# Optimization experiments

Hardware: AMD Instinct MI355X
Metric: run time of the kernel (lower is better)

## Reference

```python
import jax, jax.numpy as jnp
import numpy as np

B, T, I, H, F = 32, 1024, 64, 512, 63
NEG = -1e9


def _init_params(key):
    ks = jax.random.split(key, 16)
    s = 0.02
    p = {}
    # LSTM (pytorch gate order i,f,g,o)
    p['w_ih'] = jax.random.normal(ks[0], (4 * H, I), jnp.float32) * s
    p['w_hh'] = jax.random.normal(ks[1], (4 * H, H), jnp.float32) * s
    p['b_ih'] = jnp.zeros((4 * H,), jnp.float32)
    p['b_hh'] = jnp.zeros((4 * H,), jnp.float32)
    # shared layer
    p['w_sh'] = jax.random.normal(ks[2], (H, H), jnp.float32) * s
    p['b_sh'] = jnp.zeros((H,), jnp.float32)
    # state attention: Linear(H,H) -> tanh -> Linear(H,1)
    p['w_sa'] = jax.random.normal(ks[3], (H, H), jnp.float32) * s
    p['b_sa'] = jnp.zeros((H,), jnp.float32)
    p['v_sa'] = jax.random.normal(ks[4], (1, H), jnp.float32) * s
    p['bv_sa'] = jnp.zeros((1,), jnp.float32)
    # reward attention
    p['w_ra'] = jax.random.normal(ks[5], (H, H), jnp.float32) * s
    p['b_ra'] = jnp.zeros((H,), jnp.float32)
    p['v_ra'] = jax.random.normal(ks[6], (1, H), jnp.float32) * s
    p['bv_ra'] = jnp.zeros((1,), jnp.float32)
    # heads
    p['w_st'] = jax.random.normal(ks[7], (F, H), jnp.float32) * s
    p['b_st'] = jnp.zeros((F,), jnp.float32)
    p['w_rw'] = jax.random.normal(ks[8], (1, H), jnp.float32) * s
    p['b_rw'] = jnp.zeros((1,), jnp.float32)
    return p


def setup_inputs() -> dict:
    key = jax.random.key(0)
    k1, k2, k3, kp = jax.random.split(key, 4)
    inp = {
        'x': jax.random.normal(k1, (B, T, I), jnp.float32),
        'x_lengths': jnp.full((B,), T, dtype=jnp.int64),  # full lengths: pack/pad is identity
        'h0': jax.random.normal(k2, (B, H), jnp.float32),
        'c0': jax.random.normal(k3, (B, H), jnp.float32),
    }
    inp.update(_init_params(kp))
    return inp


def _lstm(x, h0, c0, w_ih, w_hh, b_ih, b_hh):
    # x: [B,T,I] -> outputs [B,T,H], final (h,c)
    def step(carry, xt):
        h, c = carry
        gates = xt @ w_ih.T + h @ w_hh.T + b_ih + b_hh  # [B,4H]
        i, f, g, o = jnp.split(gates, 4, axis=-1)
        c = jax.nn.sigmoid(f) * c + jax.nn.sigmoid(i) * jnp.tanh(g)
        h = jax.nn.sigmoid(o) * jnp.tanh(c)
        return (h, c), h
    (hT, cT), outs = jax.lax.scan(step, (h0, c0), jnp.swapaxes(x, 0, 1))
    return jnp.swapaxes(outs, 0, 1), hT, cT


def _causal_attn(feat, w1, b1, v, bv):
    # additive attention pooling over every causal prefix, vectorized over t.
    e = jnp.tanh(feat @ w1.T + b1) @ v.T + bv        # [B,T,1]
    e = e[..., 0]                                     # [B,T]
    t = feat.shape[1]
    causal = jnp.tril(jnp.ones((t, t), bool))         # [T,T] j<=t
    logits = jnp.where(causal[None], e[:, None, :], NEG)
    w = jax.nn.softmax(logits, axis=-1)               # [B,T,T]
    return jnp.einsum('btj,bjh->bth', w, feat)        # [B,T,H]


def reference(x, x_lengths, h0, c0, w_ih, w_hh, b_ih, b_hh, w_sh, b_sh,
              w_sa, b_sa, v_sa, bv_sa, w_ra, b_ra, v_ra, bv_ra,
              w_st, b_st, w_rw, b_rw):
    r_out, hT, cT = _lstm(x, h0, c0, w_ih, w_hh, b_ih, b_hh)
    shared = r_out @ w_sh.T + b_sh                    # [B,T,H]
    state_ctx = _causal_attn(shared, w_sa, b_sa, v_sa, bv_sa)
    reward_ctx = _causal_attn(shared, w_ra, b_ra, v_ra, bv_ra)
    state_outs = state_ctx @ w_st.T + b_st            # [B,T,F]
    reward_outs = reward_ctx @ w_rw.T + b_rw          # [B,T,1]
    return state_outs, reward_outs, (hT, cT)
```

## Files before the change

### kernel.cpp

```cpp
#include <hip/hip_runtime.h>

#define BB 32
#define TT 1024
#define II 64
#define HH 512
#define FF 63
#define G4H 2048
#define KK 576
#define MM 32768

#define RW_OFF 2064384
#define HT_OFF 2097152
#define CT_OFF 2113536

#define WS_FLAGS   0
#define WS_FLAG    4096
#define WS_TICK    4224
#define WS_CHOSEN  4288
#define WS_BIASC   4352
#define WS_BSH     12544
#define WS_BCSA    14592
#define WS_BCRA    16640
#define WS_BCH     18688
#define WS_SCAL    18944
#define WS_VS      19072
#define WS_VR      20096
#define WS_ZB      21120
#define WS_H0      23168
#define WS_CP      88704
#define WS_WHPAD   121472
#define WS_WHC     252544
#define WS_WSHT    383616
#define WS_WSA     907904
#define WS_WRA     1432192
#define WS_WCSA    1956480
#define WS_WCRA    2480768
#define WS_WCAT    3005056
#define WS_XP      5364352
#define WS_ES      9558656
#define WS_ER      9689728
#define WS_PROJ    9820800
#define WS_HX      14015104

typedef __bf16  bf16x8 __attribute__((ext_vector_type(8)));
typedef float   f32x4  __attribute__((ext_vector_type(4)));
typedef unsigned int u32x4v __attribute__((ext_vector_type(4)));
typedef uint4 uint4a __attribute__((may_alias));
typedef unsigned int u32;

#define POLL_SENTINEL 0x7FFFFFFFu

__device__ __forceinline__ float bf2f(unsigned short u) {
    unsigned int v = ((unsigned int)u) << 16;
    return __builtin_bit_cast(float, v);
}
__device__ __forceinline__ unsigned short f2bf(float f) {
    unsigned int u = __builtin_bit_cast(unsigned int, f);
    u += 0x7fffu + ((u >> 16) & 1u);
    return (unsigned short)(u >> 16);
}
__device__ __forceinline__ bf16x8 ldb8(const unsigned short* p) {
    uint4 v = *(const uint4a*)p;
    return __builtin_bit_cast(bf16x8, v);
}
__device__ __forceinline__ float sigf(float x) { return 1.f / (1.f + __expf(-x)); }
__device__ __forceinline__ float tanhfast(float x) { return 1.f - 2.f / (__expf(2.f * x) + 1.f); }

__device__ __forceinline__ unsigned short loadu(const void* p, int i, int fl) {
    return fl ? f2bf(((const float*)p)[i]) : ((const unsigned short*)p)[i];
}
__device__ __forceinline__ float loadf(const void* p, int i, int fl) {
    return fl ? ((const float*)p)[i] : bf2f(((const unsigned short*)p)[i]);
}

__global__ void sniff_k(const unsigned short* __restrict__ xr, unsigned int* __restrict__ flag) {
    if (threadIdx.x == 0) {
        int cnt = 0;
        for (int i = 0; i < 256; ++i) {
            unsigned short u = xr[i];
            int e = (u >> 7) & 0xFF;
            if (u == 0 || (e >= 100 && e <= 140)) ++cnt;
        }
        *flag = (cnt < 220) ? 1u : 0u;
    }
}

__global__ void prep_all(const void* x, const void* h0, const void* c0,
                         const void* w_sh, const void* w_sa, const void* w_ra,
                         const void* w_st, const void* w_rw,
                         const void* v_sa, const void* v_ra,
                         const void* b_sh, const void* bv_sa, const void* bv_ra,
                         char* ws) {
    const int fl = (int)*(const unsigned int*)(ws + WS_FLAG);
    unsigned short* xp    = (unsigned short*)(ws + WS_XP);
    unsigned short* h0s   = (unsigned short*)(ws + WS_H0);
    unsigned short* cp    = (unsigned short*)(ws + WS_CP);
    unsigned short* wshT  = (unsigned short*)(ws + WS_WSHT);
    unsigned short* wsa   = (unsigned short*)(ws + WS_WSA);
    unsigned short* wra   = (unsigned short*)(ws + WS_WRA);
    unsigned short* whpad = (unsigned short*)(ws + WS_WHPAD);
    unsigned short* vs    = (unsigned short*)(ws + WS_VS);
    unsigned short* vr    = (unsigned short*)(ws + WS_VR);
    float* bsh  = (float*)(ws + WS_BSH);
    float* scal = (float*)(ws + WS_SCAL);
    float* zb   = (float*)(ws + WS_ZB);

    int gt = blockIdx.x * 256 + threadIdx.x;
    int gs = gridDim.x * 256;
    for (int i = gt; i < BB * TT * II; i += gs) xp[i] = loadu(x, i, fl);
    for (int i = gt; i < BB * HH; i += gs) { h0s[i] = loadu(h0, i, fl); cp[i] = loadu(c0, i, fl); }
    for (int i = gt; i < HH * HH; i += gs) {
        int m = i >> 9, k = i & 511;
        wshT[k * HH + m] = loadu(w_sh, i, fl);
        wsa[i] = loadu(w_sa, i, fl);
        wra[i] = loadu(w_ra, i, fl);
    }
    for (int i = gt; i < 128 * HH; i += gs) {
        int f = i >> 9, k = i & 511;
        whpad[i] = (f < FF) ? loadu(w_st, f * HH + k, fl)
                 : (f == FF ? loadu(w_rw, k, fl) : (unsigned short)0);
    }
    for (int i = gt; i < HH; i += gs) {
        vs[i] = loadu(v_sa, i, fl); vr[i] = loadu(v_ra, i, fl);
        bsh[i] = loadf(b_sh, i, fl); zb[i] = 0.f;
    }
    if (gt == 0) { scal[0] = loadf(bv_sa, 0, fl); scal[1] = loadf(bv_ra, 0, fl); }
}

__global__ void prep_w(const void* __restrict__ w_hh, const void* __restrict__ w_ih,
                       const void* __restrict__ b_ih, const void* __restrict__ b_hh,
                       char* ws) {
    const int fl = (int)*(const unsigned int*)(ws + WS_FLAG);
    unsigned short* wcat = (unsigned short*)(ws + WS_WCAT);
    float* biasc = (float*)(ws + WS_BIASC);
    int c = blockIdx.x;
    for (int k = threadIdx.x; k < KK; k += 256)
        wcat[c * KK + k] = (k < HH) ? loadu(w_hh, c * HH + k, fl)
                                    : loadu(w_ih, c * II + (k - HH), fl);
    if (threadIdx.x == 0) biasc[c] = loadf(b_ih, c, fl) + loadf(b_hh, c, fl);
}

__global__ void bias_comb(const void* b_sa, const void* b_ra,
                          const void* b_st, const void* b_rw, char* ws) {
    const int fl = (int)*(const unsigned int*)(ws + WS_FLAG);
    const float* bsh = (const float*)(ws + WS_BSH);
    int j = threadIdx.x;
    if (blockIdx.x == 0) {
        const unsigned short* w = (const unsigned short*)(ws + WS_WSA);
        float s = loadf(b_sa, j, fl);
        for (int k = 0; k < HH; ++k) s += bf2f(w[j * HH + k]) * bsh[k];
        ((float*)(ws + WS_BCSA))[j] = s;
    } else if (blockIdx.x == 1) {
        const unsigned short* w = (const unsigned short*)(ws + WS_WRA);
        float s = loadf(b_ra, j, fl);
        for (int k = 0; k < HH; ++k) s += bf2f(w[j * HH + k]) * bsh[k];
        ((float*)(ws + WS_BCRA))[j] = s;
    } else if (j < 64) {
        const unsigned short* w = (const unsigned short*)(ws + WS_WHPAD);
        float s = (j < FF) ? loadf(b_st, j, fl) : loadf(b_rw, 0, fl);
        for (int k = 0; k < HH; ++k) s += bf2f(w[j * HH + k]) * bsh[k];
        ((float*)(ws + WS_BCH))[j] = s;
    }
}

__global__ void init_e(char* ws) {
    const float* scal = (const float*)(ws + WS_SCAL);
    float* es = (float*)(ws + WS_ES);
    float* er = (float*)(ws + WS_ER);
    int i = blockIdx.x * 256 + threadIdx.x;
    if (i < MM) { es[i] = scal[0]; er[i] = scal[1]; }
}

__global__ __launch_bounds__(256, 1)
void lstm_k(char* __restrict__ ws, void* __restrict__ dout) {
    __shared__ float gbuf[32][68];
    __shared__ int s_slot;
    __shared__ int s_dead;

    u32* tick   = (u32*)(ws + WS_TICK);
    u32* chosen = (u32*)(ws + WS_CHOSEN);

    if (threadIdx.x == 0) {
        u32 xcc;
        asm volatile("s_getreg_b32 %0, hwreg(HW_REG_XCC_ID)" : "=s"(xcc));
        xcc &= 7u;
        int slot = -1;
        u32 tk = __hip_atomic_fetch_add(&tick[xcc], 1u, __ATOMIC_RELAXED,
                                        __HIP_MEMORY_SCOPE_AGENT);
        if (tk < (u32)BB) {
            if (tk == (u32)BB - 1u) {
                u32 expected = 0u;
                __hip_atomic_compare_exchange_strong(chosen, &expected, xcc + 1u,
                    __ATOMIC_RELAXED, __ATOMIC_RELAXED, __HIP_MEMORY_SCOPE_AGENT);
            }
            u32 c = 0u;
            for (int it = 0; it < (1 << 20); ++it) {
                c = __hip_atomic_load(chosen, __ATOMIC_RELAXED, __HIP_MEMORY_SCOPE_AGENT);
                if (c != 0u) break;
                __builtin_amdgcn_s_sleep(8);
            }
            if (c == xcc + 1u) slot = (int)tk;
        }
        s_slot = slot;
        s_dead = 0;
    }
    __syncthreads();
    const int g = s_slot;
    if (g < 0) return;

    const unsigned short* xp    = (const unsigned short*)(ws + WS_XP);
    const unsigned short* wcat  = (const unsigned short*)(ws + WS_WCAT);
    const float*          biasc = (const float*)(ws + WS_BIASC);
    const unsigned short* cinit = (const unsigned short*)(ws + WS_CP);
    const unsigned short* h0s   = (const unsigned short*)(ws + WS_H0);
    unsigned short*       hx    = (unsigned short*)(ws + WS_HX);
    u32*                  flags = (u32*)(ws + WS_FLAGS);
    const int fl = (int)*(const unsigned int*)(ws + WS_FLAG);

    const int tid  = threadIdx.x;
    const int wave = tid >> 6, lane = tid & 63;
    const int quad = lane >> 4, l16 = lane & 15;
    const int mh = wave & 1, nh = wave >> 1;
    const int m = mh * 16 + l16;

    bf16x8 bw[2][18];
#pragma unroll
    for (int tn = 0; tn < 2; ++tn) {
        int nl   = nh * 32 + tn * 16 + l16;
        int gcol = (nl >> 4) * HH + g * 16 + (nl & 15);
        const unsigned short* wp = wcat + gcol * KK + quad * 8;
#pragma unroll
        for (int ks = 0; ks < 18; ++ks) bw[tn][ks] = ldb8(wp + ks * 32);
    }
#pragma unroll
    for (int tn = 0; tn < 2; ++tn)
#pragma unroll
        for (int ks = 0; ks < 18; ++ks) {
            u32x4v tmp = __builtin_bit_cast(u32x4v, bw[tn][ks]);
            asm volatile("" : "+v"(tmp));
            bw[tn][ks] = __builtin_bit_cast(bf16x8, tmp);
        }

    const int b  = tid >> 3, pr = tid & 7, cc = pr * 2;
    const int n  = g * 16 + cc;
    const float bi0 = biasc[n],          bi1 = biasc[n + 1];
    const float bff0 = biasc[HH + n],    bff1 = biasc[HH + n + 1];
    const float bg0 = biasc[2*HH + n],   bg1 = biasc[2*HH + n + 1];
    const float bo0 = biasc[3*HH + n],   bo1 = biasc[3*HH + n + 1];
    float cst0 = bf2f(cinit[b * HH + n]);
    float cst1 = bf2f(cinit[b * HH + n + 1]);

    const unsigned short* xbase = xp + m * (TT * II) + quad * 8;
    bf16x8 ax0 = ldb8(xbase), ax1 = ldb8(xbase + 32);

    u32* myflag = flags + g * 32;
    u32* pollp  = flags + (lane & 31) * 32;

    for (int t = 0; t < TT; ++t) {
        int tn1 = (t + 1 < TT) ? t + 1 : t;
        bf16x8 axn0 = ldb8(xbase + tn1 * II);
        bf16x8 axn1 = ldb8(xbase + tn1 * II + 32);

        const unsigned short* hrow =
            (t == 0 ? h0s : hx + (t - 1) * (BB * HH)) + m * HH + quad * 8;
        bf16x8 a[16];
#pragma unroll
        for (int i = 0; i < 16; ++i) a[i] = ldb8(hrow + i * 32);

        f32x4 acc0 = {0.f, 0.f, 0.f, 0.f}, acc1 = {0.f, 0.f, 0.f, 0.f};
#pragma unroll
        for (int i = 0; i < 16; ++i) {
            acc0 = __builtin_amdgcn_mfma_f32_16x16x32_bf16(a[i], bw[0][i], acc0, 0, 0, 0);
            acc1 = __builtin_amdgcn_mfma_f32_16x16x32_bf16(a[i], bw[1][i], acc1, 0, 0, 0);
        }
        acc0 = __builtin_amdgcn_mfma_f32_16x16x32_bf16(ax0, bw[0][16], acc0, 0, 0, 0);
        acc1 = __builtin_amdgcn_mfma_f32_16x16x32_bf16(ax0, bw[1][16], acc1, 0, 0, 0);
        acc0 = __builtin_amdgcn_mfma_f32_16x16x32_bf16(ax1, bw[0][17], acc0, 0, 0, 0);
        acc1 = __builtin_amdgcn_mfma_f32_16x16x32_bf16(ax1, bw[1][17], acc1, 0, 0, 0);

        {
            int row = mh * 16 + quad * 4;
#pragma unroll
            for (int r = 0; r < 4; ++r) gbuf[row + r][nh * 32 + l16]      = acc0[r];
#pragma unroll
            for (int r = 0; r < 4; ++r) gbuf[row + r][nh * 32 + 16 + l16] = acc1[r];
        }
        __syncthreads();

        {
            float2 giv = *(const float2*)&gbuf[b][cc];
            float2 gfv = *(const float2*)&gbuf[b][16 + cc];
            float2 ggv = *(const float2*)&gbuf[b][32 + cc];
            float2 gov = *(const float2*)&gbuf[b][48 + cc];
            cst0 = sigf(gfv.x + bff0) * cst0 + sigf(giv.x + bi0) * tanhfast(ggv.x + bg0);
            cst1 = sigf(gfv.y + bff1) * cst1 + sigf(giv.y + bi1) * tanhfast(ggv.y + bg1);
            float h0v = sigf(gov.x + bo0) * tanhfast(cst0);
            float h1v = sigf(gov.y + bo1) * tanhfast(cst1);
            u32 hp = (u32)f2bf(h0v) | ((u32)f2bf(h1v) << 16);
            *(u32*)&hx[t * (BB * HH) + b * HH + n] = hp;
            if (t == TT - 1) {
                if (fl) {
                    ((float*)dout)[HT_OFF + b * HH + n]     = h0v;
                    ((float*)dout)[HT_OFF + b * HH + n + 1] = h1v;
                    ((float*)dout)[CT_OFF + b * HH + n]     = cst0;
                    ((float*)dout)[CT_OFF + b * HH + n + 1] = cst1;
                } else {
                    ((u32*)dout)[(HT_OFF + b * HH + n) >> 1] = hp;
                    ((u32*)dout)[(CT_OFF + b * HH + n) >> 1] =
                        (u32)f2bf(cst0) | ((u32)f2bf(cst1) << 16);
                }
            }
        }
        __syncthreads();

        if (tid == 0)
            (void)__hip_atomic_fetch_add(myflag, 1u, __ATOMIC_RELAXED,
                                         __HIP_MEMORY_SCOPE_WORKGROUP);

        if (wave == 0) {
            u32 tgt = (u32)(t + 1);
            int trip = 0;
            for (int it = 0;; ++it) {
                u32 v = POLL_SENTINEL;
                __hip_atomic_compare_exchange_strong(pollp, &v, POLL_SENTINEL,
                    __ATOMIC_RELAXED, __ATOMIC_RELAXED, __HIP_MEMORY_SCOPE_WORKGROUP);
                if (__all((int)(v >= tgt && v != POLL_SENTINEL))) break;
                if (it > (1 << 16)) { trip = 1; break; }
                __builtin_amdgcn_s_sleep(1);
            }
            if (trip && lane == 0) s_dead = 1;
        }
        __syncthreads();
        if (s_dead) break;
        asm volatile("" ::: "memory");
        ax0 = axn0; ax1 = axn1;
    }
}

template <int EPI>
__global__ __launch_bounds__(256)
void gemm_bt(const unsigned short* __restrict__ A,
             const unsigned short* __restrict__ W,
             const float* __restrict__ bias,
             void* __restrict__ Cv, int N,
             const unsigned short* __restrict__ vv,
             float* __restrict__ eout) {
    __shared__ unsigned short As[128][72];
    __shared__ unsigned short Bs[64][72];
    const int tid = threadIdx.x;
    const int wave = tid >> 6, lane = tid & 63, quad = lane >> 4, l16 = lane & 15;
    const int mb = blockIdx.x, nb = blockIdx.y;

    f32x4 acc[2][4];
#pragma unroll
    for (int tm = 0; tm < 2; ++tm)
#pragma unroll
        for (int tn = 0; tn < 4; ++tn) acc[tm][tn] = (f32x4){0.f, 0.f, 0.f, 0.f};

    for (int k0 = 0; k0 < 512; k0 += 64) {
#pragma unroll
        for (int i = 0; i < 4; ++i) {
            int v = tid + i * 256;
            int rowa = v >> 3, kc = (v & 7) * 8;
            *(uint4a*)&As[rowa][kc] = *(const uint4a*)(A + (mb * 128 + rowa) * 512 + k0 + kc);
        }
#pragma unroll
        for (int i = 0; i < 2; ++i) {
            int v = tid + i * 256;
            int rowb = v >> 3, kc = (v & 7) * 8;
            *(uint4a*)&Bs[rowb][kc] = *(const uint4a*)(W + (nb * 64 + rowb) * 512 + k0 + kc);
        }
        __syncthreads();
#pragma unroll
        for (int ks = 0; ks < 2; ++ks) {
            bf16x8 a0 = ldb8(&As[wave * 32 + l16][ks * 32 + quad * 8]);
            bf16x8 a1 = ldb8(&As[wave * 32 + 16 + l16][ks * 32 + quad * 8]);
#pragma unroll
            for (int tn = 0; tn < 4; ++tn) {
                bf16x8 bb = ldb8(&Bs[tn * 16 + l16][ks * 32 + quad * 8]);
                acc[0][tn] = __builtin_amdgcn_mfma_f32_16x16x32_bf16(a0, bb, acc[0][tn], 0, 0, 0);
                acc[1][tn] = __builtin_amdgcn_mfma_f32_16x16x32_bf16(a1, bb, acc[1][tn], 0, 0, 0);
            }
        }
        __syncthreads();
    }
    if (EPI == 0) {
#pragma unroll
        for (int tm = 0; tm < 2; ++tm)
#pragma unroll
            for (int tn = 0; tn < 4; ++tn)
#pragma unroll
                for (int r = 0; r < 4; ++r) {
                    int row = mb * 128 + wave * 32 + tm * 16 + quad * 4 + r;
                    int col = nb * 64 + tn * 16 + l16;
                    ((unsigned short*)Cv)[row * N + col] = f2bf(acc[tm][tn][r] + bias[col]);
                }
    } else {
        float vcol[4], bcol[4];
#pragma unroll
        for (int tn = 0; tn < 4; ++tn) {
            int col = nb * 64 + tn * 16 + l16;
            vcol[tn] = bf2f(vv[col]); bcol[tn] = bias[col];
        }
#pragma unroll
        for (int tm = 0; tm < 2; ++tm)
#pragma unroll
            for (int r = 0; r < 4; ++r) {
                float s = 0.f;
#pragma unroll
                for (int tn = 0; tn < 4; ++tn)
                    s += vcol[tn] * tanhfast(acc[tm][tn][r] + bcol[tn]);
                s += __shfl_xor(s, 1); s += __shfl_xor(s, 2);
                s += __shfl_xor(s, 4); s += __shfl_xor(s, 8);
                if (l16 == 0) {
                    int row = mb * 128 + wave * 32 + tm * 16 + quad * 4 + r;
                    atomicAdd(&eout[row], s);
                }
            }
    }
}

__global__ __launch_bounds__(64)
void cumsum_k(char* __restrict__ ws, void* __restrict__ dout) {
    const unsigned short* proj = (const unsigned short*)(ws + WS_PROJ);
    const float* es = (const float*)(ws + WS_ES);
    const float* er = (const float*)(ws + WS_ER);
    const int fl = (int)*(const unsigned int*)(ws + WS_FLAG);
    const int b = blockIdx.x, lane = threadIdx.x;
    const bool isr = (lane == 63);
    float m_ = -3e38f, d_ = 0.f, n_ = 0.f;
    float pj = bf2f(proj[b * 64 + lane]);
    float e  = isr ? er[b] : es[b];
    for (int t = 0; t < TT; ++t) {
        float pjn = 0.f, en = 0.f;
        if (t + 1 < TT) {
            int rn = (t + 1) * BB + b;
            pjn = bf2f(proj[rn * 64 + lane]);
            en  = isr ? er[rn] : es[rn];
        }
        float mn = fmaxf(m_, e);
        float al = __expf(m_ - mn);
        float p  = __expf(e - mn);
        d_ = d_ * al + p;
        n_ = n_ * al + p * pj;
        m_ = mn;
        float o = n_ / d_;
        int rout = b * TT + t;
        int addr = isr ? (RW_OFF + rout) : (rout * FF + lane);
        if (fl) ((float*)dout)[addr] = o;
        else    ((unsigned short*)dout)[addr] = f2bf(o);
        pj = pjn; e = en;
    }
}

extern "C" void kernel_launch(void* const* d_in, const int* in_sizes, int n_in,
                              void* d_out, int out_size, void* d_ws, size_t ws_size,
                              hipStream_t stream) {
    const void* x    = d_in[0];
    const void* h0   = d_in[2];
    const void* c0   = d_in[3];
    const void* w_ih = d_in[4];
    const void* w_hh = d_in[5];
    const void* b_ih = d_in[6];
    const void* b_hh = d_in[7];
    const void* w_sh = d_in[8];
    const void* b_sh = d_in[9];
    const void* w_sa = d_in[10];
    const void* b_sa = d_in[11];
    const void* v_sa = d_in[12];
    const void* bv_sa= d_in[13];
    const void* w_ra = d_in[14];
    const void* b_ra = d_in[15];
    const void* v_ra = d_in[16];
    const void* bv_ra= d_in[17];
    const void* w_st = d_in[18];
    const void* b_st = d_in[19];
    const void* w_rw = d_in[20];
    const void* b_rw = d_in[21];

    char* ws = (char*)d_ws;
    unsigned short* wsa   = (unsigned short*)(ws + WS_WSA);
    unsigned short* wra   = (unsigned short*)(ws + WS_WRA);
    unsigned short* whpad = (unsigned short*)(ws + WS_WHPAD);
    unsigned short* wshT  = (unsigned short*)(ws + WS_WSHT);
    unsigned short* wcsa  = (unsigned short*)(ws + WS_WCSA);
    unsigned short* wcra  = (unsigned short*)(ws + WS_WCRA);
    unsigned short* whc   = (unsigned short*)(ws + WS_WHC);
    unsigned short* routs = (unsigned short*)(ws + WS_HX);
    unsigned short* proj  = (unsigned short*)(ws + WS_PROJ);
    unsigned short* vs    = (unsigned short*)(ws + WS_VS);
    unsigned short* vr    = (unsigned short*)(ws + WS_VR);
    float* zb   = (float*)(ws + WS_ZB);
    float* bcsa = (float*)(ws + WS_BCSA);
    float* bcra = (float*)(ws + WS_BCRA);
    float* bch  = (float*)(ws + WS_BCH);
    float* es   = (float*)(ws + WS_ES);
    float* er   = (float*)(ws + WS_ER);

    (void)hipMemsetAsync(d_ws, 0, 4352, stream);
    sniff_k<<<1, 64, 0, stream>>>((const unsigned short*)x, (unsigned int*)(ws + WS_FLAG));
    prep_all<<<1024, 256, 0, stream>>>(x, h0, c0, w_sh, w_sa, w_ra, w_st, w_rw,
                                       v_sa, v_ra, b_sh, bv_sa, bv_ra, ws);
    prep_w<<<G4H, 256, 0, stream>>>(w_hh, w_ih, b_ih, b_hh, ws);

    lstm_k<<<256, 256, 0, stream>>>(ws, d_out);

    gemm_bt<0><<<dim3(4, 8), 256, 0, stream>>>(wsa,   wshT, zb, wcsa, 512, nullptr, nullptr);
    gemm_bt<0><<<dim3(4, 8), 256, 0, stream>>>(wra,   wshT, zb, wcra, 512, nullptr, nullptr);
    gemm_bt<0><<<dim3(1, 8), 256, 0, stream>>>(whpad, wshT, zb, whc,  512, nullptr, nullptr);
    bias_comb<<<3, 512, 0, stream>>>(b_sa, b_ra, b_st, b_rw, ws);
    init_e<<<MM / 256, 256, 0, stream>>>(ws);

    gemm_bt<2><<<dim3(MM / 128, 8), 256, 0, stream>>>(routs, wcsa, bcsa, nullptr, 512, vs, es);
    gemm_bt<2><<<dim3(MM / 128, 8), 256, 0, stream>>>(routs, wcra, bcra, nullptr, 512, vr, er);
    gemm_bt<0><<<dim3(MM / 128, 1), 256, 0, stream>>>(routs, whc, bch, proj, 64, nullptr, nullptr);
    cumsum_k<<<BB, 64, 0, stream>>>(ws, d_out);
}
```

Before: 4.940 ms.

## Halve LSTM workgroups to 16 with wider column slices and merge attention GEMMs

The persistent LSTM now runs on 16 workgroups instead of 32, each computing 32 hidden units (128 gate columns) with four MFMA accumulators and twice the register-resident weights. This cuts the number of flag-polling peers in the per-step cross-workgroup barrier, removes the sleep in the poll loop, and signals a dead flag on timeout. Each thread now updates two cell pairs per step, so there is more serial work per workgroup and higher register pressure. The two attention-score GEMMs are merged into one launch with 16 column blocks, which relies on adjacent workspace layout of the weights, biases and score buffers. init_e is moved earlier in the launch order.

```diff
diff --git a/kernel.cpp b/kernel.cpp
--- a/kernel.cpp
+++ b/kernel.cpp
@@ -8,6 +8,7 @@
 #define G4H 2048
 #define KK 576
 #define MM 32768
+#define NW 16
 
 #define RW_OFF 2064384
 #define HT_OFF 2097152
@@ -44,7 +45,6 @@
 
 typedef __bf16  bf16x8 __attribute__((ext_vector_type(8)));
 typedef float   f32x4  __attribute__((ext_vector_type(4)));
-typedef unsigned int u32x4v __attribute__((ext_vector_type(4)));
 typedef uint4 uint4a __attribute__((may_alias));
 typedef unsigned int u32;
 
@@ -173,7 +173,7 @@
 
 __global__ __launch_bounds__(256, 1)
 void lstm_k(char* __restrict__ ws, void* __restrict__ dout) {
-    __shared__ float gbuf[32][68];
+    __shared__ float gbuf[32][132];
     __shared__ int s_slot;
     __shared__ int s_dead;
 
@@ -187,8 +187,8 @@
         int slot = -1;
         u32 tk = __hip_atomic_fetch_add(&tick[xcc], 1u, __ATOMIC_RELAXED,
                                         __HIP_MEMORY_SCOPE_AGENT);
-        if (tk < (u32)BB) {
-            if (tk == (u32)BB - 1u) {
+        if (tk < (u32)NW) {
+            if (tk == (u32)NW - 1u) {
                 u32 expected = 0u;
                 __hip_atomic_compare_exchange_strong(chosen, &expected, xcc + 1u,
                     __ATOMIC_RELAXED, __ATOMIC_RELAXED, __HIP_MEMORY_SCOPE_AGENT);
@@ -223,38 +223,35 @@
     const int mh = wave & 1, nh = wave >> 1;
     const int m = mh * 16 + l16;
 
-    bf16x8 bw[2][18];
-#pragma unroll
-    for (int tn = 0; tn < 2; ++tn) {
-        int nl   = nh * 32 + tn * 16 + l16;
-        int gcol = (nl >> 4) * HH + g * 16 + (nl & 15);
+    bf16x8 bw[4][18];
+#pragma unroll
+    for (int tn = 0; tn < 4; ++tn) {
+        int nl   = nh * 64 + tn * 16 + l16;
+        int gcol = (nl >> 5) * HH + g * 32 + (nl & 31);
         const unsigned short* wp = wcat + gcol * KK + quad * 8;
 #pragma unroll
         for (int ks = 0; ks < 18; ++ks) bw[tn][ks] = ldb8(wp + ks * 32);
     }
-#pragma unroll
-    for (int tn = 0; tn < 2; ++tn)
-#pragma unroll
-        for (int ks = 0; ks < 18; ++ks) {
-            u32x4v tmp = __builtin_bit_cast(u32x4v, bw[tn][ks]);
-            asm volatile("" : "+v"(tmp));
-            bw[tn][ks] = __builtin_bit_cast(bf16x8, tmp);
-        }
-
-    const int b  = tid >> 3, pr = tid & 7, cc = pr * 2;
-    const int n  = g * 16 + cc;
-    const float bi0 = biasc[n],          bi1 = biasc[n + 1];
-    const float bff0 = biasc[HH + n],    bff1 = biasc[HH + n + 1];
-    const float bg0 = biasc[2*HH + n],   bg1 = biasc[2*HH + n + 1];
-    const float bo0 = biasc[3*HH + n],   bo1 = biasc[3*HH + n + 1];
-    float cst0 = bf2f(cinit[b * HH + n]);
-    float cst1 = bf2f(cinit[b * HH + n + 1]);
+
+    const int b0 = tid >> 4,          cc0 = (tid & 15) * 2;
+    const int b1 = (tid + 256) >> 4,  cc1 = ((tid + 256) & 15) * 2;
+    const int n0 = g * 32 + cc0, n1 = g * 32 + cc1;
+    const float bi0a = biasc[n0],        bi0b = biasc[n0 + 1];
+    const float bf0a = biasc[HH + n0],   bf0b = biasc[HH + n0 + 1];
+    const float bg0a = biasc[2*HH + n0], bg0b = biasc[2*HH + n0 + 1];
+    const float bo0a = biasc[3*HH + n0], bo0b = biasc[3*HH + n0 + 1];
+    const float bi1a = biasc[n1],        bi1b = biasc[n1 + 1];
+    const float bf1a = biasc[HH + n1],   bf1b = biasc[HH + n1 + 1];
+    const float bg1a = biasc[2*HH + n1], bg1b = biasc[2*HH + n1 + 1];
+    const float bo1a = biasc[3*HH + n1], bo1b = biasc[3*HH + n1 + 1];
+    float cst0a = bf2f(cinit[b0 * HH + n0]), cst0b = bf2f(cinit[b0 * HH + n0 + 1]);
+    float cst1a = bf2f(cinit[b1 * HH + n1]), cst1b = bf2f(cinit[b1 * HH + n1 + 1]);
 
     const unsigned short* xbase = xp + m * (TT * II) + quad * 8;
     bf16x8 ax0 = ldb8(xbase), ax1 = ldb8(xbase + 32);
 
     u32* myflag = flags + g * 32;
-    u32* pollp  = flags + (lane & 31) * 32;
+    u32* pollp  = flags + (lane & (NW - 1)) * 32;
 
     for (int t = 0; t < TT; ++t) {
         int tn1 = (t + 1 < TT) ? t + 1 : t;
@@ -263,51 +260,82 @@
 
         const unsigned short* hrow =
             (t == 0 ? h0s : hx + (t - 1) * (BB * HH)) + m * HH + quad * 8;
-        bf16x8 a[16];
-#pragma unroll
-        for (int i = 0; i < 16; ++i) a[i] = ldb8(hrow + i * 32);
-
-        f32x4 acc0 = {0.f, 0.f, 0.f, 0.f}, acc1 = {0.f, 0.f, 0.f, 0.f};
-#pragma unroll
-        for (int i = 0; i < 16; ++i) {
-            acc0 = __builtin_amdgcn_mfma_f32_16x16x32_bf16(a[i], bw[0][i], acc0, 0, 0, 0);
-            acc1 = __builtin_amdgcn_mfma_f32_16x16x32_bf16(a[i], bw[1][i], acc1, 0, 0, 0);
-        }
-        acc0 = __builtin_amdgcn_mfma_f32_16x16x32_bf16(ax0, bw[0][16], acc0, 0, 0, 0);
-        acc1 = __builtin_amdgcn_mfma_f32_16x16x32_bf16(ax0, bw[1][16], acc1, 0, 0, 0);
-        acc0 = __builtin_amdgcn_mfma_f32_16x16x32_bf16(ax1, bw[0][17], acc0, 0, 0, 0);
-        acc1 = __builtin_amdgcn_mfma_f32_16x16x32_bf16(ax1, bw[1][17], acc1, 0, 0, 0);
+        f32x4 acc[4];
+#pragma unroll
+        for (int tn = 0; tn < 4; ++tn) acc[tn] = (f32x4){0.f, 0.f, 0.f, 0.f};
+#pragma unroll
+        for (int hf = 0; hf < 2; ++hf) {
+            bf16x8 a[8];
+#pragma unroll
+            for (int i = 0; i < 8; ++i) a[i] = ldb8(hrow + (hf * 8 + i) * 32);
+#pragma unroll
+            for (int i = 0; i < 8; ++i)
+#pragma unroll
+                for (int tn = 0; tn < 4; ++tn)
+                    acc[tn] = __builtin_amdgcn_mfma_f32_16x16x32_bf16(
+                        a[i], bw[tn][hf * 8 + i], acc[tn], 0, 0, 0);
+        }
+#pragma unroll
+        for (int tn = 0; tn < 4; ++tn) {
+            acc[tn] = __builtin_amdgcn_mfma_f32_16x16x32_bf16(ax0, bw[tn][16], acc[tn], 0, 0, 0);
+            acc[tn] = __builtin_amdgcn_mfma_f32_16x16x32_bf16(ax1, bw[tn][17], acc[tn], 0, 0, 0);
+        }
 
         {
             int row = mh * 16 + quad * 4;
 #pragma unroll
-            for (int r = 0; r < 4; ++r) gbuf[row + r][nh * 32 + l16]      = acc0[r];
-#pragma unroll
-            for (int r = 0; r < 4; ++r) gbuf[row + r][nh * 32 + 16 + l16] = acc1[r];
+            for (int tn = 0; tn < 4; ++tn)
+#pragma unroll
+                for (int r = 0; r < 4; ++r)
+                    gbuf[row + r][nh * 64 + tn * 16 + l16] = acc[tn][r];
         }
         __syncthreads();
 
         {
-            float2 giv = *(const float2*)&gbuf[b][cc];
-            float2 gfv = *(const float2*)&gbuf[b][16 + cc];
-            float2 ggv = *(const float2*)&gbuf[b][32 + cc];
-            float2 gov = *(const float2*)&gbuf[b][48 + cc];
-            cst0 = sigf(gfv.x + bff0) * cst0 + sigf(giv.x + bi0) * tanhfast(ggv.x + bg0);
-            cst1 = sigf(gfv.y + bff1) * cst1 + sigf(giv.y + bi1) * tanhfast(ggv.y + bg1);
-            float h0v = sigf(gov.x + bo0) * tanhfast(cst0);
-            float h1v = sigf(gov.y + bo1) * tanhfast(cst1);
-            u32 hp = (u32)f2bf(h0v) | ((u32)f2bf(h1v) << 16);
-            *(u32*)&hx[t * (BB * HH) + b * HH + n] = hp;
+            float2 gi = *(const float2*)&gbuf[b0][cc0];
+            float2 gf = *(const float2*)&gbuf[b0][32 + cc0];
+            float2 gg = *(const float2*)&gbuf[b0][64 + cc0];
+            float2 go = *(const float2*)&gbuf[b0][96 + cc0];
+            cst0a = sigf(gf.x + bf0a) * cst0a + sigf(gi.x + bi0a) * tanhfast(gg.x + bg0a);
+            cst0b = sigf(gf.y + bf0b) * cst0b + sigf(gi.y + bi0b) * tanhfast(gg.y + bg0b);
+            float ha = sigf(go.x + bo0a) * tanhfast(cst0a);
+            float hb = sigf(go.y + bo0b) * tanhfast(cst0b);
+            u32 hp = (u32)f2bf(ha) | ((u32)f2bf(hb) << 16);
+            *(u32*)&hx[t * (BB * HH) + b0 * HH + n0] = hp;
             if (t == TT - 1) {
                 if (fl) {
-                    ((float*)dout)[HT_OFF + b * HH + n]     = h0v;
-                    ((float*)dout)[HT_OFF + b * HH + n + 1] = h1v;
-                    ((float*)dout)[CT_OFF + b * HH + n]     = cst0;
-                    ((float*)dout)[CT_OFF + b * HH + n + 1] = cst1;
+                    ((float*)dout)[HT_OFF + b0 * HH + n0]     = ha;
+                    ((float*)dout)[HT_OFF + b0 * HH + n0 + 1] = hb;
+                    ((float*)dout)[CT_OFF + b0 * HH + n0]     = cst0a;
+                    ((float*)dout)[CT_OFF + b0 * HH + n0 + 1] = cst0b;
                 } else {
-                    ((u32*)dout)[(HT_OFF + b * HH + n) >> 1] = hp;
-                    ((u32*)dout)[(CT_OFF + b * HH + n) >> 1] =
-                        (u32)f2bf(cst0) | ((u32)f2bf(cst1) << 16);
+                    ((u32*)dout)[(HT_OFF + b0 * HH + n0) >> 1] = hp;
+                    ((u32*)dout)[(CT_OFF + b0 * HH + n0) >> 1] =
+                        (u32)f2bf(cst0a) | ((u32)f2bf(cst0b) << 16);
+                }
+            }
+        }
+        {
+            float2 gi = *(const float2*)&gbuf[b1][cc1];
+            float2 gf = *(const float2*)&gbuf[b1][32 + cc1];
+            float2 gg = *(const float2*)&gbuf[b1][64 + cc1];
+            float2 go = *(const float2*)&gbuf[b1][96 + cc1];
+            cst1a = sigf(gf.x + bf1a) * cst1a + sigf(gi.x + bi1a) * tanhfast(gg.x + bg1a);
+            cst1b = sigf(gf.y + bf1b) * cst1b + sigf(gi.y + bi1b) * tanhfast(gg.y + bg1b);
+            float ha = sigf(go.x + bo1a) * tanhfast(cst1a);
+            float hb = sigf(go.y + bo1b) * tanhfast(cst1b);
+            u32 hp = (u32)f2bf(ha) | ((u32)f2bf(hb) << 16);
+            *(u32*)&hx[t * (BB * HH) + b1 * HH + n1] = hp;
+            if (t == TT - 1) {
+                if (fl) {
+                    ((float*)dout)[HT_OFF + b1 * HH + n1]     = ha;
+                    ((float*)dout)[HT_OFF + b1 * HH + n1 + 1] = hb;
+                    ((float*)dout)[CT_OFF + b1 * HH + n1]     = cst1a;
+                    ((float*)dout)[CT_OFF + b1 * HH + n1 + 1] = cst1b;
+                } else {
+                    ((u32*)dout)[(HT_OFF + b1 * HH + n1) >> 1] = hp;
+                    ((u32*)dout)[(CT_OFF + b1 * HH + n1) >> 1] =
+                        (u32)f2bf(cst1a) | ((u32)f2bf(cst1b) << 16);
                 }
             }
         }
@@ -321,14 +349,20 @@
             u32 tgt = (u32)(t + 1);
             int trip = 0;
             for (int it = 0;; ++it) {
-                u32 v = POLL_SENTINEL;
-                __hip_atomic_compare_exchange_strong(pollp, &v, POLL_SENTINEL,
-                    __ATOMIC_RELAXED, __ATOMIC_RELAXED, __HIP_MEMORY_SCOPE_WORKGROUP);
+                u32 v = tgt;
+                if (lane < NW) {
+                    v = POLL_SENTINEL;
+                    __hip_atomic_compare_exchange_strong(pollp, &v, POLL_SENTINEL,
+                        __ATOMIC_RELAXED, __ATOMIC_RELAXED, __HIP_MEMORY_SCOPE_WORKGROUP);
+                }
                 if (__all((int)(v >= tgt && v != POLL_SENTINEL))) break;
-                if (it > (1 << 16)) { trip = 1; break; }
-                __builtin_amdgcn_s_sleep(1);
-            }
-            if (trip && lane == 0) s_dead = 1;
+                if (it > (1 << 13)) { trip = 1; break; }
+            }
+            if (trip && lane == 0) {
+                __hip_atomic_store(myflag, (u32)(TT + 2), __ATOMIC_RELAXED,
+                                   __HIP_MEMORY_SCOPE_WORKGROUP);
+                s_dead = 1;
+            }
         }
         __syncthreads();
         if (s_dead) break;
@@ -396,6 +430,7 @@
                     ((unsigned short*)Cv)[row * N + col] = f2bf(acc[tm][tn][r] + bias[col]);
                 }
     } else {
+        const int eoff = (nb >= 8) ? MM : 0;
         float vcol[4], bcol[4];
 #pragma unroll
         for (int tn = 0; tn < 4; ++tn) {
@@ -414,7 +449,7 @@
                 s += __shfl_xor(s, 4); s += __shfl_xor(s, 8);
                 if (l16 == 0) {
                     int row = mb * 128 + wave * 32 + tm * 16 + quad * 4 + r;
-                    atomicAdd(&eout[row], s);
+                    atomicAdd(&eout[eoff + row], s);
                 }
             }
     }
@@ -489,19 +524,17 @@
     unsigned short* routs = (unsigned short*)(ws + WS_HX);
     unsigned short* proj  = (unsigned short*)(ws + WS_PROJ);
     unsigned short* vs    = (unsigned short*)(ws + WS_VS);
-    unsigned short* vr    = (unsigned short*)(ws + WS_VR);
     float* zb   = (float*)(ws + WS_ZB);
     float* bcsa = (float*)(ws + WS_BCSA);
-    float* bcra = (float*)(ws + WS_BCRA);
     float* bch  = (float*)(ws + WS_BCH);
     float* es   = (float*)(ws + WS_ES);
-    float* er   = (float*)(ws + WS_ER);
 
     (void)hipMemsetAsync(d_ws, 0, 4352, stream);
     sniff_k<<<1, 64, 0, stream>>>((const unsigned short*)x, (unsigned int*)(ws + WS_FLAG));
     prep_all<<<1024, 256, 0, stream>>>(x, h0, c0, w_sh, w_sa, w_ra, w_st, w_rw,
                                        v_sa, v_ra, b_sh, bv_sa, bv_ra, ws);
     prep_w<<<G4H, 256, 0, stream>>>(w_hh, w_ih, b_ih, b_hh, ws);
+    init_e<<<MM / 256, 256, 0, stream>>>(ws);
 
     lstm_k<<<256, 256, 0, stream>>>(ws, d_out);
 
@@ -509,10 +542,8 @@
     gemm_bt<0><<<dim3(4, 8), 256, 0, stream>>>(wra,   wshT, zb, wcra, 512, nullptr, nullptr);
     gemm_bt<0><<<dim3(1, 8), 256, 0, stream>>>(whpad, wshT, zb, whc,  512, nullptr, nullptr);
     bias_comb<<<3, 512, 0, stream>>>(b_sa, b_ra, b_st, b_rw, ws);
-    init_e<<<MM / 256, 256, 0, stream>>>(ws);
-
-    gemm_bt<2><<<dim3(MM / 128, 8), 256, 0, stream>>>(routs, wcsa, bcsa, nullptr, 512, vs, es);
-    gemm_bt<2><<<dim3(MM / 128, 8), 256, 0, stream>>>(routs, wcra, bcra, nullptr, 512, vr, er);
+
+    gemm_bt<2><<<dim3(MM / 128, 16), 256, 0, stream>>>(routs, wcsa, bcsa, nullptr, 512, vs, es);
     gemm_bt<0><<<dim3(MM / 128, 1), 256, 0, stream>>>(routs, whc, bch, proj, 64, nullptr, nullptr);
     cumsum_k<<<BB, 64, 0, stream>>>(ws, d_out);
 }
```

New measurement: 5.324 ms. 1.08x slower.

## Replace per-step LSTM barrier with fine-grained per-chunk flag polling and merge attention GEMMs

Applied to the files above, without the earlier changes.

The persistent LSTM kernel drops the end-of-step wave-0 spin barrier and its second __syncthreads. Instead, each h-chunk load waits only until the producer blocks for that chunk have published step t. The input-projection MFMAs are moved ahead so they overlap the wait, and a failed wait now marks the flag so other blocks stop. Separately, the two attention-score GEMMs are merged into one launch with a doubled grid that relies on the wcsa/wcra and es/er buffers being contiguous, and init_e is hoisted before the LSTM; the tighter handshake risks subtle ordering or visibility races.

```diff
diff --git a/kernel.cpp b/kernel.cpp
--- a/kernel.cpp
+++ b/kernel.cpp
@@ -8,6 +8,7 @@
 #define G4H 2048
 #define KK 576
 #define MM 32768
+#define NW 32
 
 #define RW_OFF 2064384
 #define HT_OFF 2097152
@@ -44,9 +45,9 @@
 
 typedef __bf16  bf16x8 __attribute__((ext_vector_type(8)));
 typedef float   f32x4  __attribute__((ext_vector_type(4)));
-typedef unsigned int u32x4v __attribute__((ext_vector_type(4)));
 typedef uint4 uint4a __attribute__((may_alias));
 typedef unsigned int u32;
+typedef unsigned long long u64;
 
 #define POLL_SENTINEL 0x7FFFFFFFu
 
@@ -187,8 +188,8 @@
         int slot = -1;
         u32 tk = __hip_atomic_fetch_add(&tick[xcc], 1u, __ATOMIC_RELAXED,
                                         __HIP_MEMORY_SCOPE_AGENT);
-        if (tk < (u32)BB) {
-            if (tk == (u32)BB - 1u) {
+        if (tk < (u32)NW) {
+            if (tk == (u32)NW - 1u) {
                 u32 expected = 0u;
                 __hip_atomic_compare_exchange_strong(chosen, &expected, xcc + 1u,
                     __ATOMIC_RELAXED, __ATOMIC_RELAXED, __HIP_MEMORY_SCOPE_AGENT);
@@ -232,14 +233,6 @@
 #pragma unroll
         for (int ks = 0; ks < 18; ++ks) bw[tn][ks] = ldb8(wp + ks * 32);
     }
-#pragma unroll
-    for (int tn = 0; tn < 2; ++tn)
-#pragma unroll
-        for (int ks = 0; ks < 18; ++ks) {
-            u32x4v tmp = __builtin_bit_cast(u32x4v, bw[tn][ks]);
-            asm volatile("" : "+v"(tmp));
-            bw[tn][ks] = __builtin_bit_cast(bf16x8, tmp);
-        }
 
     const int b  = tid >> 3, pr = tid & 7, cc = pr * 2;
     const int n  = g * 16 + cc;
@@ -263,20 +256,35 @@
 
         const unsigned short* hrow =
             (t == 0 ? h0s : hx + (t - 1) * (BB * HH)) + m * HH + quad * 8;
+        const u32 tgt = (u32)t;
+        u64 ball = 0;
+        int it = 0, trip = 0;
         bf16x8 a[16];
 #pragma unroll
-        for (int i = 0; i < 16; ++i) a[i] = ldb8(hrow + i * 32);
+        for (int i = 0; i < 16; ++i) {
+            while (((ball >> (2 * i)) & 3ull) != 3ull) {
+                u32 v = 0xFFFFFFFFu;
+                if (lane < 32) {
+                    v = POLL_SENTINEL;
+                    __hip_atomic_compare_exchange_strong(pollp, &v, POLL_SENTINEL,
+                        __ATOMIC_RELAXED, __ATOMIC_RELAXED, __HIP_MEMORY_SCOPE_WORKGROUP);
+                }
+                ball = __ballot(v >= tgt && v != POLL_SENTINEL);
+                if (++it > (1 << 16)) { trip = 1; ball = ~0ull; }
+            }
+            a[i] = ldb8(hrow + i * 32);
+        }
 
         f32x4 acc0 = {0.f, 0.f, 0.f, 0.f}, acc1 = {0.f, 0.f, 0.f, 0.f};
-#pragma unroll
-        for (int i = 0; i < 16; ++i) {
-            acc0 = __builtin_amdgcn_mfma_f32_16x16x32_bf16(a[i], bw[0][i], acc0, 0, 0, 0);
-            acc1 = __builtin_amdgcn_mfma_f32_16x16x32_bf16(a[i], bw[1][i], acc1, 0, 0, 0);
-        }
         acc0 = __builtin_amdgcn_mfma_f32_16x16x32_bf16(ax0, bw[0][16], acc0, 0, 0, 0);
         acc1 = __builtin_amdgcn_mfma_f32_16x16x32_bf16(ax0, bw[1][16], acc1, 0, 0, 0);
         acc0 = __builtin_amdgcn_mfma_f32_16x16x32_bf16(ax1, bw[0][17], acc0, 0, 0, 0);
         acc1 = __builtin_amdgcn_mfma_f32_16x16x32_bf16(ax1, bw[1][17], acc1, 0, 0, 0);
+#pragma unroll
+        for (int i = 0; i < 16; ++i) {
+            acc0 = __builtin_amdgcn_mfma_f32_16x16x32_bf16(a[i], bw[0][i], acc0, 0, 0, 0);
+            acc1 = __builtin_amdgcn_mfma_f32_16x16x32_bf16(a[i], bw[1][i], acc1, 0, 0, 0);
+        }
 
         {
             int row = mh * 16 + quad * 4;
@@ -285,6 +293,7 @@
 #pragma unroll
             for (int r = 0; r < 4; ++r) gbuf[row + r][nh * 32 + 16 + l16] = acc1[r];
         }
+        if (trip) s_dead = 1;
         __syncthreads();
 
         {
@@ -313,26 +322,15 @@
         }
         __syncthreads();
 
-        if (tid == 0)
-            (void)__hip_atomic_fetch_add(myflag, 1u, __ATOMIC_RELAXED,
-                                         __HIP_MEMORY_SCOPE_WORKGROUP);
-
-        if (wave == 0) {
-            u32 tgt = (u32)(t + 1);
-            int trip = 0;
-            for (int it = 0;; ++it) {
-                u32 v = POLL_SENTINEL;
-                __hip_atomic_compare_exchange_strong(pollp, &v, POLL_SENTINEL,
-                    __ATOMIC_RELAXED, __ATOMIC_RELAXED, __HIP_MEMORY_SCOPE_WORKGROUP);
-                if (__all((int)(v >= tgt && v != POLL_SENTINEL))) break;
-                if (it > (1 << 16)) { trip = 1; break; }
-                __builtin_amdgcn_s_sleep(1);
-            }
-            if (trip && lane == 0) s_dead = 1;
-        }
-        __syncthreads();
+        if (tid == 0) {
+            if (s_dead)
+                __hip_atomic_store(myflag, (u32)(TT + 2), __ATOMIC_RELAXED,
+                                   __HIP_MEMORY_SCOPE_WORKGROUP);
+            else
+                (void)__hip_atomic_fetch_add(myflag, 1u, __ATOMIC_RELAXED,
+                                             __HIP_MEMORY_SCOPE_WORKGROUP);
+        }
         if (s_dead) break;
-        asm volatile("" ::: "memory");
         ax0 = axn0; ax1 = axn1;
     }
 }
@@ -396,6 +394,7 @@
                     ((unsigned short*)Cv)[row * N + col] = f2bf(acc[tm][tn][r] + bias[col]);
                 }
     } else {
+        const int eoff = (nb >= 8) ? MM : 0;
         float vcol[4], bcol[4];
 #pragma unroll
         for (int tn = 0; tn < 4; ++tn) {
@@ -414,7 +413,7 @@
                 s += __shfl_xor(s, 4); s += __shfl_xor(s, 8);
                 if (l16 == 0) {
                     int row = mb * 128 + wave * 32 + tm * 16 + quad * 4 + r;
-                    atomicAdd(&eout[row], s);
+                    atomicAdd(&eout[eoff + row], s);
                 }
             }
     }
@@ -484,35 +483,31 @@
     unsigned short* whpad = (unsigned short*)(ws + WS_WHPAD);
     unsigned short* wshT  = (unsigned short*)(ws + WS_WSHT);
     unsigned short* wcsa  = (unsigned short*)(ws + WS_WCSA);
-    unsigned short* wcra  = (unsigned short*)(ws + WS_WCRA);
     unsigned short* whc   = (unsigned short*)(ws + WS_WHC);
     unsigned short* routs = (unsigned short*)(ws + WS_HX);
     unsigned short* proj  = (unsigned short*)(ws + WS_PROJ);
     unsigned short* vs    = (unsigned short*)(ws + WS_VS);
-    unsigned short* vr    = (unsigned short*)(ws + WS_VR);
     float* zb   = (float*)(ws + WS_ZB);
     float* bcsa = (float*)(ws + WS_BCSA);
-    float* bcra = (float*)(ws + WS_BCRA);
     float* bch  = (float*)(ws + WS_BCH);
     float* es   = (float*)(ws + WS_ES);
-    float* er   = (float*)(ws + WS_ER);
 
     (void)hipMemsetAsync(d_ws, 0, 4352, stream);
     sniff_k<<<1, 64, 0, stream>>>((const unsigned short*)x, (unsigned int*)(ws + WS_FLAG));
     prep_all<<<1024, 256, 0, stream>>>(x, h0, c0, w_sh, w_sa, w_ra, w_st, w_rw,
                                        v_sa, v_ra, b_sh, bv_sa, bv_ra, ws);
     prep_w<<<G4H, 256, 0, stream>>>(w_hh, w_ih, b_ih, b_hh, ws);
+    init_e<<<MM / 256, 256, 0, stream>>>(ws);
 
     lstm_k<<<256, 256, 0, stream>>>(ws, d_out);
 
     gemm_bt<0><<<dim3(4, 8), 256, 0, stream>>>(wsa,   wshT, zb, wcsa, 512, nullptr, nullptr);
-    gemm_bt<0><<<dim3(4, 8), 256, 0, stream>>>(wra,   wshT, zb, wcra, 512, nullptr, nullptr);
+    gemm_bt<0><<<dim3(4, 8), 256, 0, stream>>>(wra,   wshT, zb,
+                                               (unsigned short*)(ws + WS_WCRA), 512, nullptr, nullptr);
     gemm_bt<0><<<dim3(1, 8), 256, 0, stream>>>(whpad, wshT, zb, whc,  512, nullptr, nullptr);
     bias_comb<<<3, 512, 0, stream>>>(b_sa, b_ra, b_st, b_rw, ws);
-    init_e<<<MM / 256, 256, 0, stream>>>(ws);
-
-    gemm_bt<2><<<dim3(MM / 128, 8), 256, 0, stream>>>(routs, wcsa, bcsa, nullptr, 512, vs, es);
-    gemm_bt<2><<<dim3(MM / 128, 8), 256, 0, stream>>>(routs, wcra, bcra, nullptr, 512, vr, er);
+
+    gemm_bt<2><<<dim3(MM / 128, 16), 256, 0, stream>>>(routs, wcsa, bcsa, nullptr, 512, vs, es);
     gemm_bt<0><<<dim3(MM / 128, 1), 256, 0, stream>>>(routs, whc, bch, proj, 64, nullptr, nullptr);
     cumsum_k<<<BB, 64, 0, stream>>>(ws, d_out);
 }
```

Result: slower. 5.187 ms (+5.0%).
